# Optimization experiments

Measured on AMD Instinct MI355X. Metric: run time of the kernel, lower is better.

The kernel has to match this reference:

```python
import jax, jax.numpy as jnp
import numpy as np

TIME_SEG_LEN = 5
PRED_STEPS = 1
B, N, D = 4, 4096, 4
F1, F2 = 32, 64  # cnn filters; F2 must equal GCSConv/Dense width 64


def _conv1d_time(x, Wc1, bc1, Wc2, bc2):
    # x: [B, N, T, D] -> per-node temporal CNN collapsing T=5 -> 1 -> [B, N, F2]
    b, n, t, d = x.shape
    xr = x.reshape(b * n, t, d)
    dn = ('NWC', 'WIO', 'NWC')
    h = jax.lax.conv_general_dilated(xr, Wc1, (1,), 'VALID', dimension_numbers=dn) + bc1
    h = jax.nn.relu(h)
    h = jax.lax.conv_general_dilated(h, Wc2, (1,), 'VALID', dimension_numbers=dn) + bc2
    return h.reshape(b, n, -1)  # [B, N, F2]


def setup_inputs() -> dict:
    key = jax.random.key(0)
    ks = jax.random.split(key, 12)
    time_segs = jax.random.normal(ks[0], (B, TIME_SEG_LEN, N, D), dtype=jnp.float32)
    edges = jax.random.randint(ks[1], (N, N), 0, 2, dtype=jnp.int32)
    s = lambda *sh: 1.0 / np.sqrt(sh[-2] if len(sh) > 1 else sh[0])
    return {
        'time_segs': time_segs,
        'edges': edges,
        'Wc1': jax.random.normal(ks[2], (3, D, F1), dtype=jnp.float32) * 0.3,
        'bc1': jnp.zeros((F1,), jnp.float32),
        'Wc2': jax.random.normal(ks[3], (3, F1, F2), dtype=jnp.float32) * 0.1,
        'bc2': jnp.zeros((F2,), jnp.float32),
        'Wg1': jax.random.normal(ks[4], (F2, 64), dtype=jnp.float32) * 0.125,
        'bg': jnp.zeros((64,), jnp.float32),
        'Wd': jax.random.normal(ks[5], (F2 + 64, 64), dtype=jnp.float32) * 0.09,
        'bd': jnp.zeros((64,), jnp.float32),
        'Wo': jax.random.normal(ks[6], (64, D), dtype=jnp.float32) * 0.125,
        'bo': jnp.zeros((D,), jnp.float32),
    }


def reference(time_segs, edges, Wc1, bc1, Wc2, bc2, Wg1, bg, Wd, bd, Wo, bo):
    A = edges.astype(jnp.float32)
    n = A.shape[0]
    deg = jnp.sum(A, axis=-1, keepdims=True)              # row degree
    A_norm = A / jnp.where(deg > 0, deg, 1.0)             # D^-1 A (symmetric=False)
    A_nd = A_norm * (1.0 - jnp.eye(n, dtype=A.dtype))     # self-edge masking of X row j == zeroing diag
    col_deg = jnp.sum(A, axis=0)                          # e = np.sum(edges, axis=0)
    alive = (col_deg != 0).astype(time_segs.dtype)[None, :, None]  # zero-degree nodes -> zeros branch

    ext = jnp.transpose(time_segs, (0, 2, 1, 3))          # [B, N, T, D]
    for i in range(PRED_STEPS):
        seg = ext[:, :, i:, :]                            # [B, N, 5, D]
        cond = _conv1d_time(seg, Wc1, bc1, Wc2, bc2)      # [B, N, F2]
        # Vectorized per-node masked GCSConv: row j of tanh(A X_j W1 + X_j W2 + b)
        # with X_j = X zeroed at node j. Skip term vanishes at row j.
        agg = jnp.einsum('jk,bkf->bjf', A_nd, cond)       # [B, N, F2]
        G = jnp.tanh(agg @ Wg1 + bg) * alive              # [B, N, 64]
        h = jax.nn.relu(jnp.concatenate([cond, G], axis=-1) @ Wd + bd)
        nxt = seg[:, :, -1, :] + jnp.tanh(h @ Wo + bo)    # residual update [B, N, D]
        ext = jnp.concatenate([ext, nxt[:, :, None, :]], axis=2)
    out = jnp.transpose(ext, (0, 2, 1, 3))                # [B, T+P, N, D]
    return out[:, TIME_SEG_LEN:, :, :]                    # [B, pred_steps, N, D]
```

## Files before the change

### kernel.cpp

```cpp
#include <hip/hip_runtime.h>
#include <math.h>

typedef unsigned short ushort_t;
typedef unsigned int uint_t;
typedef unsigned long long u64_t;
typedef __attribute__((ext_vector_type(8))) __bf16 bf16x8;
typedef __attribute__((ext_vector_type(4))) float f32x4;

#define NN 4096
#define TT 5
#define F1 32
#define F2 64

__device__ __forceinline__ ushort_t f2bf(float x) {
    union { float f; uint_t u; } v; v.f = x;
    uint_t r = (v.u + 0x7FFFu + ((v.u >> 16) & 1u)) >> 16;
    return (ushort_t)r;
}
__device__ __forceinline__ float bf16f(float x) {
    union { float f; uint_t u; } v; v.f = x;
    v.u = (v.u + 0x7FFFu + ((v.u >> 16) & 1u)) & 0xFFFF0000u;
    return v.f;
}
__device__ __forceinline__ uint_t pk2(float a, float b) {
    return (uint_t)f2bf(a) | ((uint_t)f2bf(b) << 16);
}
__device__ __forceinline__ float tanh_fast(float x) {
    const float xc = fminf(fmaxf(x, -10.f), 10.f);
    const float e = __expf(2.f * xc);
    return (e - 1.f) * __builtin_amdgcn_rcpf(e + 1.f);
}
__device__ __forceinline__ void lds_barrier() {
    asm volatile("s_waitcnt lgkmcnt(0)\n\ts_barrier" ::: "memory");
}

#define H1S 104
#define CBS 80
__global__ __launch_bounds__(512) void k1_cond(
    const float* __restrict__ ts, const float* __restrict__ Wc1, const float* __restrict__ bc1,
    const float* __restrict__ Wc2, const float* __restrict__ bc2,
    float* __restrict__ condf, ushort_t* __restrict__ condT,
    int* __restrict__ degI, uint_t* __restrict__ colbits)
{
    const int b = blockIdx.y;
    const int j0 = blockIdx.x * 64;
    const int t = threadIdx.x;

    __shared__ float sWc1[384];
    __shared__ float sbc1[F1];
    __shared__ float sbc2[F2];
    __shared__ ushort_t sWc2T[64 * H1S];
    __shared__ ushort_t h1B[64 * H1S];
    __shared__ ushort_t scb[64 * CBS];

    if (blockIdx.x == 0 && b == 0) {
        for (int i = t; i < 4096; i += 512) degI[i] = 0;
        if (t < 128) colbits[t] = 0u;
    }

    for (int i = t; i < 384; i += 512) sWc1[i] = Wc1[i];
    if (t < F1) sbc1[t] = bc1[t];
    if (t < F2) sbc2[t] = bc2[t];
    for (int i = t; i < 96 * 64; i += 512) {
        const int e = i >> 6, f = i & 63;
        sWc2T[f * H1S + e] = f2bf(Wc2[i]);
    }
    __syncthreads();

    {
        const int n = t & 63, g = t >> 6;
        const int j = j0 + n;
        float4 x[5];
        #pragma unroll
        for (int tt = 0; tt < 5; ++tt)
            x[tt] = *(const float4*)(ts + ((((size_t)b * TT + tt) << 12) + j) * 4);
        #pragma unroll
        for (int q = 0; q < 12; ++q) {
            const int e = g * 12 + q;
            const int tt0 = e >> 5, f1 = e & 31;
            float a = sbc1[f1];
            #pragma unroll
            for (int dt = 0; dt < 3; ++dt) {
                const float4 xx = x[tt0 + dt];
                a += xx.x * sWc1[(dt * 4 + 0) * F1 + f1];
                a += xx.y * sWc1[(dt * 4 + 1) * F1 + f1];
                a += xx.z * sWc1[(dt * 4 + 2) * F1 + f1];
                a += xx.w * sWc1[(dt * 4 + 3) * F1 + f1];
            }
            h1B[n * H1S + e] = f2bf(fmaxf(a, 0.f));
        }
    }
    __syncthreads();

    {
        const int w = t >> 6, l = t & 63;
        const int m0 = (w & 3) * 16, cH = (w >> 2) * 32;
        const int kseg = (l >> 4) * 8;
        f32x4 acc[2] = {};
        #pragma unroll
        for (int ks = 0; ks < 3; ++ks) {
            const bf16x8 av = *(const bf16x8*)&h1B[(m0 + (l & 15)) * H1S + ks * 32 + kseg];
            #pragma unroll
            for (int ct = 0; ct < 2; ++ct) {
                const bf16x8 bv = *(const bf16x8*)&sWc2T[(cH + ct * 16 + (l & 15)) * H1S + ks * 32 + kseg];
                acc[ct] = __builtin_amdgcn_mfma_f32_16x16x32_bf16(av, bv, acc[ct], 0, 0, 0);
            }
        }
        #pragma unroll
        for (int ct = 0; ct < 2; ++ct)
            #pragma unroll
            for (int i = 0; i < 4; ++i) {
                const int row = m0 + (l >> 4) * 4 + i;
                const int col = cH + ct * 16 + (l & 15);
                const float c = acc[ct][i] + sbc2[col];
                condf[((((size_t)b << 12) + j0 + row) << 6) + col] = c;
                scb[col * CBS + row] = f2bf(c);
            }
    }
    __syncthreads();
    {
        const int f2 = t >> 3, seg = t & 7;
        ushort_t* dst = condT + (((size_t)b * 64 + f2) << 12) + j0 + seg * 8;
        *(uint4*)dst = *(const uint4*)&scb[f2 * CBS + seg * 8];
    }
}

__device__ __forceinline__ void stage_chunk(
    const int4 pa, int it, int kq, ushort_t* dstbuf, int soff, uint_t& regm, int& cnt)
{
    const u64_t b0 = __ballot(pa.x != 0);
    const u64_t b1 = __ballot(pa.y != 0);
    const u64_t b2 = __ballot(pa.z != 0);
    const u64_t b3 = __ballot(pa.w != 0);
    const uint_t m0 = (uint_t)(b0 | (b0 >> 32)), m1 = (uint_t)(b1 | (b1 >> 32));
    const uint_t m2 = (uint_t)(b2 | (b2 >> 32)), m3 = (uint_t)(b3 | (b3 >> 32));
    const uint_t nib = ((m0 >> kq) & 1u) | (((m1 >> kq) & 1u) << 1) |
                       (((m2 >> kq) & 1u) << 2) | (((m3 >> kq) & 1u) << 3);
    regm |= nib << (it * 4);
    cnt += (pa.x != 0) + (pa.y != 0) + (pa.z != 0) + (pa.w != 0);
    const uint_t h01 = (pa.x ? 0x3F80u : 0u) | (pa.y ? 0x3F800000u : 0u);
    const uint_t h23 = (pa.z ? 0x3F80u : 0u) | (pa.w ? 0x3F800000u : 0u);
    *(uint2*)(dstbuf + soff) = make_uint2(h01, h23);
}

__global__ __launch_bounds__(1024, 8) void k3_gemm(
    const int* __restrict__ edges, const ushort_t* __restrict__ condT,
    float* __restrict__ agg0, float* __restrict__ agg1,
    float* __restrict__ agg2, float* __restrict__ agg3,
    int* __restrict__ degI, uint_t* __restrict__ colbits)
{
    const int t = threadIdx.x;
    const int stripe = blockIdx.x >> 2, ks4 = blockIdx.x & 3;
    const int j0 = stripe * 32, kb = ks4 * 1024;

    __shared__ __align__(16) ushort_t abuf[8][4096];

    const int w = t >> 6, l = t & 63;
    const int r = t >> 5, kq = t & 31;
    const int rl = r & 15, rh = r >> 4;
    const int ks_s = kq >> 3, q_s = (kq >> 1) & 3;
    const int soff = (rh * 2048 + ks_s * 512 + (q_s * 16 + rl) * 8 + (kq & 1) * 4) ^ (q_s << 4);
    const int aoff = (l * 8) ^ ((l >> 4) << 4);

    const int* ep = edges + (size_t)(j0 + r) * NN + kb + kq * 4;
    const ushort_t* bp = condT + (size_t)(w * 16 + (l & 15)) * NN + kb + (l >> 4) * 8;

    uint_t regm = 0; int cnt = 0;
    int4 pa[4];
    bf16x8 bcur[4], bnxt[4];

    #pragma unroll
    for (int c = 0; c < 4; ++c) pa[c] = *(const int4*)(ep + c * 128);
    #pragma unroll
    for (int ks = 0; ks < 4; ++ks) bcur[ks] = *(const bf16x8*)(bp + ks * 32);
    #pragma unroll
    for (int c = 0; c < 4; ++c) stage_chunk(pa[c], c, kq, &abuf[c][0], soff, regm, cnt);
    lds_barrier();

    #pragma unroll
    for (int c = 0; c < 4; ++c) pa[c] = *(const int4*)(ep + (c + 4) * 128);

    f32x4 acc0 = {0.f, 0.f, 0.f, 0.f};
    f32x4 acc1 = {0.f, 0.f, 0.f, 0.f};

    #pragma unroll
    for (int ch = 0; ch < 4; ++ch) {
        const ushort_t* bpn = bp + (ch + 1) * 128;
        #pragma unroll
        for (int ks = 0; ks < 4; ++ks) bnxt[ks] = *(const bf16x8*)(bpn + ks * 32);
        const ushort_t* ab = &abuf[ch][0];
        #pragma unroll
        for (int ks = 0; ks < 4; ++ks) {
            const bf16x8 a0 = *(const bf16x8*)(ab + ks * 512 + aoff);
            const bf16x8 a1 = *(const bf16x8*)(ab + 2048 + ks * 512 + aoff);
            acc0 = __builtin_amdgcn_mfma_f32_16x16x32_bf16(a0, bcur[ks], acc0, 0, 0, 0);
            acc1 = __builtin_amdgcn_mfma_f32_16x16x32_bf16(a1, bcur[ks], acc1, 0, 0, 0);
        }
        #pragma unroll
        for (int ks = 0; ks < 4; ++ks) bcur[ks] = bnxt[ks];
    }
    #pragma unroll
    for (int c = 0; c < 4; ++c) stage_chunk(pa[c], c + 4, kq, &abuf[c + 4][0], soff, regm, cnt);
    lds_barrier();

    #pragma unroll
    for (int ch = 4; ch < 8; ++ch) {
        if (ch < 7) {
            const ushort_t* bpn = bp + (ch + 1) * 128;
            #pragma unroll
            for (int ks = 0; ks < 4; ++ks) bnxt[ks] = *(const bf16x8*)(bpn + ks * 32);
        }
        const ushort_t* ab = &abuf[ch][0];
        #pragma unroll
        for (int ks = 0; ks < 4; ++ks) {
            const bf16x8 a0 = *(const bf16x8*)(ab + ks * 512 + aoff);
            const bf16x8 a1 = *(const bf16x8*)(ab + 2048 + ks * 512 + aoff);
            acc0 = __builtin_amdgcn_mfma_f32_16x16x32_bf16(a0, bcur[ks], acc0, 0, 0, 0);
            acc1 = __builtin_amdgcn_mfma_f32_16x16x32_bf16(a1, bcur[ks], acc1, 0, 0, 0);
        }
        if (ch < 7) {
            #pragma unroll
            for (int ks = 0; ks < 4; ++ks) bcur[ks] = bnxt[ks];
        }
    }

    {
        float* aggS = (ks4 == 0) ? agg0 : (ks4 == 1) ? agg1 : (ks4 == 2) ? agg2 : agg3;
        const int col = w * 16 + (l & 15);
        float* dst = aggS + ((size_t)(col >> 6) * NN << 6) + (col & 63);
        #pragma unroll
        for (int i = 0; i < 4; ++i) {
            const int ja = j0 + (l >> 4) * 4 + i;
            dst[(size_t)ja << 6] = acc0[i];
            dst[(size_t)(ja + 16) << 6] = acc1[i];
        }
    }
    {
        int s = cnt;
        #pragma unroll
        for (int off = 16; off >= 1; off >>= 1) s += __shfl_down(s, off, 32);
        if (kq == 0) atomicAdd(&degI[j0 + r], s);
    }
    __syncthreads();
    uint_t* colsh = (uint_t*)&abuf[0][0];
    if (l < 32) colsh[w * 32 + kq] = regm;
    __syncthreads();
    if (t < 32) {
        uint_t v = 0;
        #pragma unroll
        for (int w2 = 0; w2 < 16; ++w2) v |= colsh[w2 * 32 + t];
        colsh[512 + t] = v;
    }
    __syncthreads();
    if (t < 32) {
        const int it = t >> 2, koct = t & 3;
        uint_t word = 0;
        #pragma unroll
        for (int s2 = 0; s2 < 8; ++s2)
            word |= ((colsh[512 + koct * 8 + s2] >> (it * 4)) & 15u) << (s2 * 4);
        atomicOr(&colbits[(kb >> 5) + t], word);
    }
}

#define WGS 88
#define WDS 136
#define HS  69
__global__ __launch_bounds__(512) void k4_mlp(
    const float* __restrict__ ts, const int* __restrict__ edges,
    const float* __restrict__ condf,
    const float* __restrict__ agg0, const float* __restrict__ agg1,
    const float* __restrict__ agg2, const float* __restrict__ agg3,
    const int* __restrict__ degI, const uint_t* __restrict__ colbits,
    const float* __restrict__ Wg1, const float* __restrict__ bg,
    const float* __restrict__ Wd, const float* __restrict__ bd,
    const float* __restrict__ Wo, const float* __restrict__ bo,
    float* __restrict__ out)
{
    const int b = blockIdx.y;
    const int j0 = blockIdx.x * 64;
    const int t = threadIdx.x;

    __shared__ ushort_t sWg1T[64 * WGS];
    __shared__ ushort_t sWdT[64 * WDS];
    __shared__ ushort_t aggB[64 * WGS];
    __shared__ ushort_t catB[64 * WDS];
    __shared__ float sH[64 * HS];
    __shared__ float sWo[256];
    __shared__ float sbg[64], sbd[64], sbo[4], sAlive[64];

    for (int i = t; i < 4096; i += 512) {
        const int in = i >> 6, o = i & 63;
        sWg1T[o * WGS + in] = f2bf(Wg1[i]);
    }
    for (int i = t; i < 8192; i += 512) {
        const int in = i >> 6, o = i & 63;
        sWdT[o * WDS + in] = f2bf(Wd[i]);
    }
    if (t < 256) sWo[t] = Wo[t];
    if (t >= 256 && t < 320) { sbg[t - 256] = bg[t - 256]; sbd[t - 256] = bd[t - 256]; }
    if (t >= 320 && t < 324) sbo[t - 320] = bo[t - 320];
    if (t >= 384 && t < 448) {
        const int j = j0 + t - 384;
        sAlive[t - 384] = (float)((colbits[j >> 5] >> (j & 31)) & 1u);
    }
    {
        const int r = t >> 3, fs = t & 7;
        const int j = j0 + r;
        const float dv = (float)degI[j];
        const float inv = 1.f / (dv > 0.f ? dv : 1.f);
        const float dgf = edges[(size_t)j * NN + j] ? 1.f : 0.f;
        const size_t base = (((size_t)b << 12) + j) << 6;
        #pragma unroll
        for (int q = 0; q < 2; ++q) {
            const int f = fs * 8 + q * 4;
            const float4 a0 = *(const float4*)(agg0 + base + f);
            const float4 a1 = *(const float4*)(agg1 + base + f);
            const float4 a2 = *(const float4*)(agg2 + base + f);
            const float4 a3 = *(const float4*)(agg3 + base + f);
            const float4 c4 = *(const float4*)(condf + base + f);
            const float n0 = (a0.x + a1.x + a2.x + a3.x - dgf * bf16f(c4.x)) * inv;
            const float n1 = (a0.y + a1.y + a2.y + a3.y - dgf * bf16f(c4.y)) * inv;
            const float n2 = (a0.z + a1.z + a2.z + a3.z - dgf * bf16f(c4.z)) * inv;
            const float n3 = (a0.w + a1.w + a2.w + a3.w - dgf * bf16f(c4.w)) * inv;
            *(uint2*)&aggB[r * WGS + f] = make_uint2(pk2(n0, n1), pk2(n2, n3));
            *(uint2*)&catB[r * WDS + f] = make_uint2(pk2(c4.x, c4.y), pk2(c4.z, c4.w));
        }
    }
    __syncthreads();

    const int w = t >> 6, l = t & 63;
    const int m0 = (w & 3) * 16, cH = (w >> 2) * 32;
    const int kseg = (l >> 4) * 8;

    {
        f32x4 acc[2] = {};
        #pragma unroll
        for (int ks = 0; ks < 2; ++ks) {
            const bf16x8 av = *(const bf16x8*)&aggB[(m0 + (l & 15)) * WGS + ks * 32 + kseg];
            #pragma unroll
            for (int ct = 0; ct < 2; ++ct) {
                const bf16x8 bv = *(const bf16x8*)&sWg1T[(cH + ct * 16 + (l & 15)) * WGS + ks * 32 + kseg];
                acc[ct] = __builtin_amdgcn_mfma_f32_16x16x32_bf16(av, bv, acc[ct], 0, 0, 0);
            }
        }
        #pragma unroll
        for (int ct = 0; ct < 2; ++ct)
            #pragma unroll
            for (int i = 0; i < 4; ++i) {
                const int row = m0 + (l >> 4) * 4 + i;
                const int col = cH + ct * 16 + (l & 15);
                const float g = tanh_fast(acc[ct][i] + sbg[col]) * sAlive[row];
                catB[row * WDS + 64 + col] = f2bf(g);
            }
    }
    __syncthreads();
    {
        f32x4 acc[2] = {};
        #pragma unroll
        for (int ks = 0; ks < 4; ++ks) {
            const bf16x8 av = *(const bf16x8*)&catB[(m0 + (l & 15)) * WDS + ks * 32 + kseg];
            #pragma unroll
            for (int ct = 0; ct < 2; ++ct) {
                const bf16x8 bv = *(const bf16x8*)&sWdT[(cH + ct * 16 + (l & 15)) * WDS + ks * 32 + kseg];
                acc[ct] = __builtin_amdgcn_mfma_f32_16x16x32_bf16(av, bv, acc[ct], 0, 0, 0);
            }
        }
        #pragma unroll
        for (int ct = 0; ct < 2; ++ct)
            #pragma unroll
            for (int i = 0; i < 4; ++i) {
                const int row = m0 + (l >> 4) * 4 + i;
                const int col = cH + ct * 16 + (l & 15);
                sH[row * HS + col] = fmaxf(acc[ct][i] + sbd[col], 0.f);
            }
    }
    __syncthreads();
    if (t < 256) {
        const int r = t >> 2, d = t & 3;
        const int j = j0 + r;
        float s = sbo[d];
        #pragma unroll 8
        for (int f = 0; f < 64; ++f) s += sH[r * HS + f] * sWo[f * 4 + d];
        const float segl = ts[((((size_t)b * TT + 4) << 12) + j) * 4 + d];
        out[((((size_t)b << 12) + j) << 2) + d] = segl + tanh_fast(s);
    }
}

extern "C" void kernel_launch(void* const* d_in, const int* in_sizes, int n_in,
                              void* d_out, int out_size, void* d_ws, size_t ws_size,
                              hipStream_t stream)
{
    (void)in_sizes; (void)n_in; (void)out_size; (void)ws_size;
    const float* ts    = (const float*)d_in[0];
    const int*   edges = (const int*)d_in[1];
    const float* Wc1   = (const float*)d_in[2];
    const float* bc1   = (const float*)d_in[3];
    const float* Wc2   = (const float*)d_in[4];
    const float* bc2   = (const float*)d_in[5];
    const float* Wg1   = (const float*)d_in[6];
    const float* bg    = (const float*)d_in[7];
    const float* Wd    = (const float*)d_in[8];
    const float* bd    = (const float*)d_in[9];
    const float* Wo    = (const float*)d_in[10];
    const float* bo    = (const float*)d_in[11];
    float* out = (float*)d_out;

    char* ws = (char*)d_ws;
    ushort_t* condT   = (ushort_t*)(ws);
    float*    condf   = (float*)(ws + (size_t)(2 << 20));
    float*    agg0    = (float*)(ws + (size_t)(6 << 20));
    float*    agg1    = (float*)(ws + (size_t)(10 << 20));
    float*    agg2    = (float*)(ws + (size_t)(14 << 20));
    float*    agg3    = (float*)(ws + (size_t)(18 << 20));
    int*      degI    = (int*)(ws + (size_t)(22 << 20));
    uint_t*   colbits = (uint_t*)(ws + (size_t)(22 << 20) + 16384);

    k1_cond<<<dim3(64, 4), 512, 0, stream>>>(ts, Wc1, bc1, Wc2, bc2, condf, condT,
                                             degI, colbits);
    k3_gemm<<<512, 1024, 0, stream>>>(edges, condT, agg0, agg1, agg2, agg3, degI, colbits);
    k4_mlp<<<dim3(64, 4), 512, 0, stream>>>(ts, edges, condf, agg0, agg1, agg2, agg3,
                                            degI, colbits, Wg1, bg, Wd, bd, Wo, bo, out);
}
```

Before: 175.6 us.

## Pre-pack adjacency into bitmask kernel and retile aggregation GEMM over all batches

Adds a k0_pack kernel that reads the int32 adjacency once and writes a 1-bit-per-edge packed matrix, plus row degrees and column-alive bits. The GEMM now reads this 2 MB bitmask instead of the 64 MB int matrix and expands bits to bf16 in LDS. It uses 128-row tiles covering all 256 output columns (every batch) with an 8-way K split into partial slabs, and k4 sums eight slabs instead of four. This adds a kernel launch, a memset and more partial-sum traffic, in exchange for removing the repeated wide edge reads and the atomics from the GEMM.

```diff
diff --git a/kernel.cpp b/kernel.cpp
--- a/kernel.cpp
+++ b/kernel.cpp
@@ -30,8 +30,65 @@
     const float e = __expf(2.f * xc);
     return (e - 1.f) * __builtin_amdgcn_rcpf(e + 1.f);
 }
-__device__ __forceinline__ void lds_barrier() {
-    asm volatile("s_waitcnt lgkmcnt(0)\n\ts_barrier" ::: "memory");
+
+__global__ __launch_bounds__(1024) void k0_pack(
+    const int* __restrict__ edges, uint_t* __restrict__ packed,
+    int* __restrict__ degI, uint_t* __restrict__ colbits)
+{
+    const int t = threadIdx.x, w = t >> 6, l = t & 63;
+    const int row = blockIdx.x * 16 + w;
+    __shared__ u64_t lmask[16][64];
+
+    const int* ep = edges + (size_t)row * NN + l * 4;
+    u64_t nib = 0; int cnt = 0;
+    #pragma unroll
+    for (int g = 0; g < 2; ++g) {
+        int4 v[8];
+        #pragma unroll
+        for (int q = 0; q < 8; ++q) v[q] = *(const int4*)(ep + (g * 8 + q) * 256);
+        #pragma unroll
+        for (int q = 0; q < 8; ++q) {
+            const uint_t n = (uint_t)(v[q].x != 0) | ((uint_t)(v[q].y != 0) << 1) |
+                             ((uint_t)(v[q].z != 0) << 2) | ((uint_t)(v[q].w != 0) << 3);
+            cnt += (v[q].x != 0) + (v[q].y != 0) + (v[q].z != 0) + (v[q].w != 0);
+            nib |= (u64_t)n << ((g * 8 + q) * 4);
+        }
+    }
+    lmask[w][l] = nib;
+    {
+        int s = cnt;
+        #pragma unroll
+        for (int off = 32; off >= 1; off >>= 1) s += __shfl_down(s, off, 64);
+        if (l == 0) degI[row] = s;
+    }
+    {
+        #pragma unroll
+        for (int h = 0; h < 2; ++h) {
+            const int w2 = l + h * 64;
+            const int q = w2 >> 3, g = w2 & 7;
+            uint_t word = 0;
+            #pragma unroll
+            for (int i = 0; i < 8; ++i)
+                word |= (uint_t)((lmask[w][g * 8 + i] >> (q * 4)) & 15ull) << (i * 4);
+            packed[(size_t)row * 128 + w2] = word;
+        }
+    }
+    __syncthreads();
+    if (t < 64) {
+        u64_t m = 0;
+        #pragma unroll
+        for (int w2 = 0; w2 < 16; ++w2) m |= lmask[w2][t];
+        lmask[0][t] = m;
+    }
+    __syncthreads();
+    if (t < 128) {
+        const int q = t >> 3, g = t & 7;
+        uint_t word = 0;
+        #pragma unroll
+        for (int i = 0; i < 8; ++i)
+            word |= (uint_t)((lmask[0][g * 8 + i] >> (q * 4)) & 15ull) << (i * 4);
+        atomicOr(&colbits[t], word);
+    }
 }
 
 #define H1S 104
@@ -39,8 +96,7 @@
 __global__ __launch_bounds__(512) void k1_cond(
     const float* __restrict__ ts, const float* __restrict__ Wc1, const float* __restrict__ bc1,
     const float* __restrict__ Wc2, const float* __restrict__ bc2,
-    float* __restrict__ condf, ushort_t* __restrict__ condT,
-    int* __restrict__ degI, uint_t* __restrict__ colbits)
+    float* __restrict__ condf, ushort_t* __restrict__ condT)
 {
     const int b = blockIdx.y;
     const int j0 = blockIdx.x * 64;
@@ -53,11 +109,6 @@
     __shared__ ushort_t h1B[64 * H1S];
     __shared__ ushort_t scb[64 * CBS];
 
-    if (blockIdx.x == 0 && b == 0) {
-        for (int i = t; i < 4096; i += 512) degI[i] = 0;
-        if (t < 128) colbits[t] = 0u;
-    }
-
     for (int i = t; i < 384; i += 512) sWc1[i] = Wc1[i];
     if (t < F1) sbc1[t] = bc1[t];
     if (t < F2) sbc2[t] = bc2[t];
@@ -125,140 +176,83 @@
     }
 }
 
-__device__ __forceinline__ void stage_chunk(
-    const int4 pa, int it, int kq, ushort_t* dstbuf, int soff, uint_t& regm, int& cnt)
-{
-    const u64_t b0 = __ballot(pa.x != 0);
-    const u64_t b1 = __ballot(pa.y != 0);
-    const u64_t b2 = __ballot(pa.z != 0);
-    const u64_t b3 = __ballot(pa.w != 0);
-    const uint_t m0 = (uint_t)(b0 | (b0 >> 32)), m1 = (uint_t)(b1 | (b1 >> 32));
-    const uint_t m2 = (uint_t)(b2 | (b2 >> 32)), m3 = (uint_t)(b3 | (b3 >> 32));
-    const uint_t nib = ((m0 >> kq) & 1u) | (((m1 >> kq) & 1u) << 1) |
-                       (((m2 >> kq) & 1u) << 2) | (((m3 >> kq) & 1u) << 3);
-    regm |= nib << (it * 4);
-    cnt += (pa.x != 0) + (pa.y != 0) + (pa.z != 0) + (pa.w != 0);
-    const uint_t h01 = (pa.x ? 0x3F80u : 0u) | (pa.y ? 0x3F800000u : 0u);
-    const uint_t h23 = (pa.z ? 0x3F80u : 0u) | (pa.w ? 0x3F800000u : 0u);
-    *(uint2*)(dstbuf + soff) = make_uint2(h01, h23);
-}
-
-__global__ __launch_bounds__(1024, 8) void k3_gemm(
-    const int* __restrict__ edges, const ushort_t* __restrict__ condT,
-    float* __restrict__ agg0, float* __restrict__ agg1,
-    float* __restrict__ agg2, float* __restrict__ agg3,
-    int* __restrict__ degI, uint_t* __restrict__ colbits)
+__global__ __launch_bounds__(1024) void k3_gemm(
+    const uint_t* __restrict__ packed, const ushort_t* __restrict__ condT,
+    float* __restrict__ aggAll)
 {
     const int t = threadIdx.x;
-    const int stripe = blockIdx.x >> 2, ks4 = blockIdx.x & 3;
-    const int j0 = stripe * 32, kb = ks4 * 1024;
-
-    __shared__ __align__(16) ushort_t abuf[8][4096];
+    const int rt = blockIdx.x >> 3, ks = blockIdx.x & 7;
+    const int j0 = rt * 128, kb = ks * 512;
+
+    __shared__ __align__(16) ushort_t abuf[2][128 * 16 * 8];
+
+    const int srow = t >> 3, koct = t & 7;
+    const uint_t* prow = packed + (size_t)(j0 + srow) * 128 + (kb >> 5);
+    const int sh = (koct & 1) * 16;
+    const int kf0 = koct * 2;
+    const int u0 = (srow * 16 + (kf0 ^ (srow & 15))) * 8;
+    const int u1 = (srow * 16 + ((kf0 + 1) ^ (srow & 15))) * 8;
 
     const int w = t >> 6, l = t & 63;
-    const int r = t >> 5, kq = t & 31;
-    const int rl = r & 15, rh = r >> 4;
-    const int ks_s = kq >> 3, q_s = (kq >> 1) & 3;
-    const int soff = (rh * 2048 + ks_s * 512 + (q_s * 16 + rl) * 8 + (kq & 1) * 4) ^ (q_s << 4);
-    const int aoff = (l * 8) ^ ((l >> 4) << 4);
-
-    const int* ep = edges + (size_t)(j0 + r) * NN + kb + kq * 4;
-    const ushort_t* bp = condT + (size_t)(w * 16 + (l & 15)) * NN + kb + (l >> 4) * 8;
-
-    uint_t regm = 0; int cnt = 0;
-    int4 pa[4];
-    bf16x8 bcur[4], bnxt[4];
-
+    const int rg = w & 7, chh = w >> 3;
+    const int arow = rg * 16 + (l & 15);
+    const int asub = l >> 4;
+    const ushort_t* bpbase = condT + (size_t)(chh * 128 + (l & 15)) * NN + kb + asub * 8;
+
+    f32x4 acc[8] = {};
+
+    {
+        const uint_t b16 = prow[koct >> 1] >> sh;
+        uint_t e[8];
+        #pragma unroll
+        for (int p = 0; p < 8; ++p)
+            e[p] = (((b16 >> (2 * p)) & 1u) ? 0x3F80u : 0u) |
+                   (((b16 >> (2 * p + 1)) & 1u) ? 0x3F800000u : 0u);
+        *(uint4*)(&abuf[0][u0]) = make_uint4(e[0], e[1], e[2], e[3]);
+        *(uint4*)(&abuf[0][u1]) = make_uint4(e[4], e[5], e[6], e[7]);
+    }
+    __syncthreads();
+
+    for (int c = 0; c < 4; ++c) {
+        uint_t wn = 0;
+        if (c < 3) wn = prow[(c + 1) * 4 + (koct >> 1)];
+        const ushort_t* ab = &abuf[c & 1][0];
+        #pragma unroll
+        for (int tt = 0; tt < 4; ++tt) {
+            const int kf = tt * 4 + asub;
+            const bf16x8 av = *(const bf16x8*)(ab + (arow * 16 + (kf ^ (arow & 15))) * 8);
+            const ushort_t* bp = bpbase + c * 128 + tt * 32;
+            #pragma unroll
+            for (int cf = 0; cf < 8; ++cf) {
+                const bf16x8 bv = *(const bf16x8*)(bp + (size_t)cf * 16 * NN);
+                acc[cf] = __builtin_amdgcn_mfma_f32_16x16x32_bf16(av, bv, acc[cf], 0, 0, 0);
+            }
+        }
+        __syncthreads();
+        if (c < 3) {
+            const uint_t b16 = wn >> sh;
+            uint_t e[8];
+            #pragma unroll
+            for (int p = 0; p < 8; ++p)
+                e[p] = (((b16 >> (2 * p)) & 1u) ? 0x3F80u : 0u) |
+                       (((b16 >> (2 * p + 1)) & 1u) ? 0x3F800000u : 0u);
+            ushort_t* bufn = &abuf[(c + 1) & 1][0];
+            *(uint4*)(bufn + u0) = make_uint4(e[0], e[1], e[2], e[3]);
+            *(uint4*)(bufn + u1) = make_uint4(e[4], e[5], e[6], e[7]);
+            __syncthreads();
+        }
+    }
+
+    float* slab = aggAll + (size_t)ks * (1 << 20);
     #pragma unroll
-    for (int c = 0; c < 4; ++c) pa[c] = *(const int4*)(ep + c * 128);
-    #pragma unroll
-    for (int ks = 0; ks < 4; ++ks) bcur[ks] = *(const bf16x8*)(bp + ks * 32);
-    #pragma unroll
-    for (int c = 0; c < 4; ++c) stage_chunk(pa[c], c, kq, &abuf[c][0], soff, regm, cnt);
-    lds_barrier();
-
-    #pragma unroll
-    for (int c = 0; c < 4; ++c) pa[c] = *(const int4*)(ep + (c + 4) * 128);
-
-    f32x4 acc0 = {0.f, 0.f, 0.f, 0.f};
-    f32x4 acc1 = {0.f, 0.f, 0.f, 0.f};
-
-    #pragma unroll
-    for (int ch = 0; ch < 4; ++ch) {
-        const ushort_t* bpn = bp + (ch + 1) * 128;
-        #pragma unroll
-        for (int ks = 0; ks < 4; ++ks) bnxt[ks] = *(const bf16x8*)(bpn + ks * 32);
-        const ushort_t* ab = &abuf[ch][0];
-        #pragma unroll
-        for (int ks = 0; ks < 4; ++ks) {
-            const bf16x8 a0 = *(const bf16x8*)(ab + ks * 512 + aoff);
-            const bf16x8 a1 = *(const bf16x8*)(ab + 2048 + ks * 512 + aoff);
-            acc0 = __builtin_amdgcn_mfma_f32_16x16x32_bf16(a0, bcur[ks], acc0, 0, 0, 0);
-            acc1 = __builtin_amdgcn_mfma_f32_16x16x32_bf16(a1, bcur[ks], acc1, 0, 0, 0);
-        }
-        #pragma unroll
-        for (int ks = 0; ks < 4; ++ks) bcur[ks] = bnxt[ks];
-    }
-    #pragma unroll
-    for (int c = 0; c < 4; ++c) stage_chunk(pa[c], c + 4, kq, &abuf[c + 4][0], soff, regm, cnt);
-    lds_barrier();
-
-    #pragma unroll
-    for (int ch = 4; ch < 8; ++ch) {
-        if (ch < 7) {
-            const ushort_t* bpn = bp + (ch + 1) * 128;
-            #pragma unroll
-            for (int ks = 0; ks < 4; ++ks) bnxt[ks] = *(const bf16x8*)(bpn + ks * 32);
-        }
-        const ushort_t* ab = &abuf[ch][0];
-        #pragma unroll
-        for (int ks = 0; ks < 4; ++ks) {
-            const bf16x8 a0 = *(const bf16x8*)(ab + ks * 512 + aoff);
-            const bf16x8 a1 = *(const bf16x8*)(ab + 2048 + ks * 512 + aoff);
-            acc0 = __builtin_amdgcn_mfma_f32_16x16x32_bf16(a0, bcur[ks], acc0, 0, 0, 0);
-            acc1 = __builtin_amdgcn_mfma_f32_16x16x32_bf16(a1, bcur[ks], acc1, 0, 0, 0);
-        }
-        if (ch < 7) {
-            #pragma unroll
-            for (int ks = 0; ks < 4; ++ks) bcur[ks] = bnxt[ks];
-        }
-    }
-
-    {
-        float* aggS = (ks4 == 0) ? agg0 : (ks4 == 1) ? agg1 : (ks4 == 2) ? agg2 : agg3;
-        const int col = w * 16 + (l & 15);
-        float* dst = aggS + ((size_t)(col >> 6) * NN << 6) + (col & 63);
+    for (int cf = 0; cf < 8; ++cf) {
+        const int col = chh * 128 + cf * 16 + (l & 15);
+        float* dst = slab + ((size_t)(col >> 6) * NN << 6) + (col & 63);
         #pragma unroll
         for (int i = 0; i < 4; ++i) {
-            const int ja = j0 + (l >> 4) * 4 + i;
-            dst[(size_t)ja << 6] = acc0[i];
-            dst[(size_t)(ja + 16) << 6] = acc1[i];
-        }
-    }
-    {
-        int s = cnt;
-        #pragma unroll
-        for (int off = 16; off >= 1; off >>= 1) s += __shfl_down(s, off, 32);
-        if (kq == 0) atomicAdd(&degI[j0 + r], s);
-    }
-    __syncthreads();
-    uint_t* colsh = (uint_t*)&abuf[0][0];
-    if (l < 32) colsh[w * 32 + kq] = regm;
-    __syncthreads();
-    if (t < 32) {
-        uint_t v = 0;
-        #pragma unroll
-        for (int w2 = 0; w2 < 16; ++w2) v |= colsh[w2 * 32 + t];
-        colsh[512 + t] = v;
-    }
-    __syncthreads();
-    if (t < 32) {
-        const int it = t >> 2, koct = t & 3;
-        uint_t word = 0;
-        #pragma unroll
-        for (int s2 = 0; s2 < 8; ++s2)
-            word |= ((colsh[512 + koct * 8 + s2] >> (it * 4)) & 15u) << (s2 * 4);
-        atomicOr(&colbits[(kb >> 5) + t], word);
+            const int j = j0 + rg * 16 + asub * 4 + i;
+            dst[(size_t)j << 6] = acc[cf][i];
+        }
     }
 }
 
@@ -267,9 +261,7 @@
 #define HS  69
 __global__ __launch_bounds__(512) void k4_mlp(
     const float* __restrict__ ts, const int* __restrict__ edges,
-    const float* __restrict__ condf,
-    const float* __restrict__ agg0, const float* __restrict__ agg1,
-    const float* __restrict__ agg2, const float* __restrict__ agg3,
+    const float* __restrict__ condf, const float* __restrict__ aggAll,
     const int* __restrict__ degI, const uint_t* __restrict__ colbits,
     const float* __restrict__ Wg1, const float* __restrict__ bg,
     const float* __restrict__ Wd, const float* __restrict__ bd,
@@ -313,15 +305,17 @@
         #pragma unroll
         for (int q = 0; q < 2; ++q) {
             const int f = fs * 8 + q * 4;
-            const float4 a0 = *(const float4*)(agg0 + base + f);
-            const float4 a1 = *(const float4*)(agg1 + base + f);
-            const float4 a2 = *(const float4*)(agg2 + base + f);
-            const float4 a3 = *(const float4*)(agg3 + base + f);
+            float4 a4 = {0.f, 0.f, 0.f, 0.f};
+            #pragma unroll
+            for (int s = 0; s < 8; ++s) {
+                const float4 sv = *(const float4*)(aggAll + (size_t)s * (1 << 20) + base + f);
+                a4.x += sv.x; a4.y += sv.y; a4.z += sv.z; a4.w += sv.w;
+            }
             const float4 c4 = *(const float4*)(condf + base + f);
-            const float n0 = (a0.x + a1.x + a2.x + a3.x - dgf * bf16f(c4.x)) * inv;
-            const float n1 = (a0.y + a1.y + a2.y + a3.y - dgf * bf16f(c4.y)) * inv;
-            const float n2 = (a0.z + a1.z + a2.z + a3.z - dgf * bf16f(c4.z)) * inv;
-            const float n3 = (a0.w + a1.w + a2.w + a3.w - dgf * bf16f(c4.w)) * inv;
+            const float n0 = (a4.x - dgf * bf16f(c4.x)) * inv;
+            const float n1 = (a4.y - dgf * bf16f(c4.y)) * inv;
+            const float n2 = (a4.z - dgf * bf16f(c4.z)) * inv;
+            const float n3 = (a4.w - dgf * bf16f(c4.w)) * inv;
             *(uint2*)&aggB[r * WGS + f] = make_uint2(pk2(n0, n1), pk2(n2, n3));
             *(uint2*)&catB[r * WDS + f] = make_uint2(pk2(c4.x, c4.y), pk2(c4.z, c4.w));
         }
@@ -408,16 +402,16 @@
     char* ws = (char*)d_ws;
     ushort_t* condT   = (ushort_t*)(ws);
     float*    condf   = (float*)(ws + (size_t)(2 << 20));
-    float*    agg0    = (float*)(ws + (size_t)(6 << 20));
-    float*    agg1    = (float*)(ws + (size_t)(10 << 20));
-    float*    agg2    = (float*)(ws + (size_t)(14 << 20));
-    float*    agg3    = (float*)(ws + (size_t)(18 << 20));
-    int*      degI    = (int*)(ws + (size_t)(22 << 20));
-    uint_t*   colbits = (uint_t*)(ws + (size_t)(22 << 20) + 16384);
-
-    k1_cond<<<dim3(64, 4), 512, 0, stream>>>(ts, Wc1, bc1, Wc2, bc2, condf, condT,
-                                             degI, colbits);
-    k3_gemm<<<512, 1024, 0, stream>>>(edges, condT, agg0, agg1, agg2, agg3, degI, colbits);
-    k4_mlp<<<dim3(64, 4), 512, 0, stream>>>(ts, edges, condf, agg0, agg1, agg2, agg3,
-                                            degI, colbits, Wg1, bg, Wd, bd, Wo, bo, out);
-}
+    float*    aggAll  = (float*)(ws + (size_t)(6 << 20));
+    uint_t*   packed  = (uint_t*)(ws + (size_t)(38 << 20));
+    int*      degI    = (int*)(ws + (size_t)(40 << 20));
+    uint_t*   colbits = (uint_t*)(ws + (size_t)(40 << 20) + 16384);
+
+    hipMemsetAsync(colbits, 0, 512, stream);
+
+    k0_pack<<<256, 1024, 0, stream>>>(edges, packed, degI, colbits);
+    k1_cond<<<dim3(64, 4), 512, 0, stream>>>(ts, Wc1, bc1, Wc2, bc2, condf, condT);
+    k3_gemm<<<256, 1024, 0, stream>>>(packed, condT, aggAll);
+    k4_mlp<<<dim3(64, 4), 512, 0, stream>>>(ts, edges, condf, aggAll, degI, colbits,
+                                            Wg1, bg, Wd, bd, Wo, bo, out);
+}
```

Result: slower. 212.5 us (+21.0%).
